# Kernel tuning notes

Measured on AMD Instinct MI355X. Metric: run time of the kernel, lower is better.

## Reference

```python
import jax, jax.numpy as jnp
import numpy as np

HEAD_SIZE = 128


def setup_inputs() -> dict:
    key = jax.random.key(0)
    k0, k1, k2, k3 = jax.random.split(key, 4)
    B, S, E, H = 4, 4096, 1024, HEAD_SIZE
    x = jax.random.normal(k0, (B, S, E), dtype=jnp.float32)
    scale = 1.0 / np.sqrt(E).astype(np.float32)
    Wq = jax.random.normal(k1, (E, H), dtype=jnp.float32) * scale
    Wk = jax.random.normal(k2, (E, H), dtype=jnp.float32) * scale
    Wv = jax.random.normal(k3, (E, H), dtype=jnp.float32) * scale
    k_mask = jnp.ones((B, S), dtype=jnp.int32)
    return {"x": x, "Wq": Wq, "Wk": Wk, "Wv": Wv, "k_mask": k_mask}


def reference(x, Wq, Wk, Wv, k_mask):
    # Self-attention path (kv=None), causal=True
    Q = x @ Wq  # [B, S, H]
    K = x @ Wk  # [B, S, H]
    V = x @ Wv  # [B, S, H]
    inv_sqrt_h = np.float32(1.0 / np.sqrt(HEAD_SIZE))
    att = jnp.einsum('bqh,bkh->bqk', Q, K) * inv_sqrt_h  # [B, S, S]
    neg_inf = jnp.float32(-jnp.inf)
    # padding mask over keys: [B, 1, S_k]
    att = jnp.where(k_mask[:, None, :] == 0, neg_inf, att)
    # causal mask: tril over (q_len, k_len)
    S = Q.shape[1]
    c_mask = jnp.tril(jnp.ones((S, S), dtype=bool))  # [S, S]
    att = jnp.where(c_mask[None, :, :], att, neg_inf)
    att = jax.nn.softmax(att, axis=-1)
    return att @ V  # [B, S, H]
```

## Files before the change

kernel.cpp:

```cpp
#include <hip/hip_runtime.h>

typedef unsigned short u16;
typedef __attribute__((ext_vector_type(8))) short bf16x8;
typedef __attribute__((ext_vector_type(4))) float f32x4;
typedef __attribute__((ext_vector_type(8))) unsigned short u16x8;
typedef __attribute__((ext_vector_type(4))) unsigned short u16x4;

#define SQ 4096
#define HQ 128
#define NCHUNKF 160

__device__ __forceinline__ u16 f2b(float f) {
  unsigned int u = __float_as_uint(f);
  unsigned int r = (u + 0x7fffu + ((u >> 16) & 1u)) >> 16;
  return (u16)r;
}

__device__ __forceinline__ void gload_lds16(const u16* gsrc, u16* ldst) {
  __builtin_amdgcn_global_load_lds((const __attribute__((address_space(1))) void*)gsrc,
                                   (__attribute__((address_space(3))) void*)ldst, 16, 0, 0);
}

__global__ __launch_bounds__(256) void k_wt(const float* __restrict__ Wq, const float* __restrict__ Wk,
                                            const float* __restrict__ Wv, u16* __restrict__ wt) {
  int idx = blockIdx.x * 256 + threadIdx.x;
  int z = idx >> 17, r = idx & 131071, n = r >> 10, k = r & 1023;
  const float* W = (z == 0) ? Wq : (z == 1) ? Wk : Wv;
  wt[idx] = f2b(W[k * 128 + n]);
}

__global__ __launch_bounds__(512, 4) void k_proj(const float* __restrict__ x, const u16* __restrict__ wt,
                                                 u16* __restrict__ qb, u16* __restrict__ kb,
                                                 u16* __restrict__ vt) {
  int blk = blockIdx.x;
  int t = threadIdx.x;
  int w = t >> 6, lane = t & 63;
  int wm = w >> 2, wn = w & 3;
  int lr = lane & 15, lg = lane >> 4;

  __shared__ __align__(16) u16 xl[2][64 * 32];
  __shared__ __align__(16) u16 wl[2][384 * 32];

  int srow = t >> 3, sc8 = t & 7;
  const float* xg = x + (long)(blk * 64 + srow) * 1024 + sc8 * 4;
  int xch = ((sc8 >> 1) ^ ((srow >> 1) & 3));
  int xoff = srow * 32 + xch * 8 + (sc8 & 1) * 4;

  f32x4 acc[2][6];
#pragma unroll
  for (int i = 0; i < 2; ++i)
#pragma unroll
    for (int j = 0; j < 6; ++j) acc[i][j] = (f32x4){0.f, 0.f, 0.f, 0.f};

  auto stage_w = [&](int bufi, int k0) {
#pragma unroll
    for (int i = 0; i < 3; ++i) {
      int ci = i * 512 + t;
      int row = ci >> 2, ch = ci & 3;
      gload_lds16(wt + (long)row * 1024 + k0 + ((ch ^ ((row >> 1) & 3)) << 3),
                  &wl[bufi][0] + ci * 8);
    }
  };

  {
    float4 xa = *(const float4*)(xg);
    stage_w(0, 0);
    u16x4 o;
    o[0] = f2b(xa.x); o[1] = f2b(xa.y); o[2] = f2b(xa.z); o[3] = f2b(xa.w);
    *(u16x4*)(&xl[0][0] + xoff) = o;
  }
  __syncthreads();

  int arow0 = wm * 32 + lr;
  for (int ks = 0; ks < 32; ++ks) {
    int cur = ks & 1;
    float4 xa;
    bool more = (ks + 1 < 32);
    if (more) {
      xa = *(const float4*)(xg + (ks + 1) * 32);
      stage_w(cur ^ 1, (ks + 1) * 32);
    }
    bf16x8 af[2], bf[6];
#pragma unroll
    for (int i = 0; i < 2; ++i) {
      int row = arow0 + i * 16;
      af[i] = *(const bf16x8*)(&xl[cur][0] + row * 32 + ((lg ^ ((row >> 1) & 3)) << 3));
    }
#pragma unroll
    for (int j = 0; j < 6; ++j) {
      int row = wn * 96 + j * 16 + lr;
      bf[j] = *(const bf16x8*)(&wl[cur][0] + row * 32 + ((lg ^ ((row >> 1) & 3)) << 3));
    }
#pragma unroll
    for (int i = 0; i < 2; ++i)
#pragma unroll
      for (int j = 0; j < 6; ++j)
        acc[i][j] = __builtin_amdgcn_mfma_f32_16x16x32_bf16(af[i], bf[j], acc[i][j], 0, 0, 0);
    if (more) {
      u16x4 o;
      o[0] = f2b(xa.x); o[1] = f2b(xa.y); o[2] = f2b(xa.z); o[3] = f2b(xa.w);
      *(u16x4*)(&xl[cur ^ 1][0] + xoff) = o;
    }
    __syncthreads();
  }

#pragma unroll
  for (int i = 0; i < 2; ++i)
#pragma unroll
    for (int j = 0; j < 6; ++j)
#pragma unroll
      for (int r = 0; r < 4; ++r) {
        int m = blk * 64 + wm * 32 + i * 16 + lg * 4 + r;
        int col = wn * 96 + j * 16 + lr;
        int z = col >> 7, cz = col & 127;
        u16 v = f2b(acc[i][j][r]);
        if (z == 0) qb[(long)m * 128 + cz] = v;
        else if (z == 1) kb[(long)m * 128 + cz] = v;
        else { int bb = m >> 12, sR = m & 4095; vt[(long)bb * 524288 + (long)cz * 4096 + sR] = v; }
      }
}

__global__ __launch_bounds__(256) void k_attn(const u16* __restrict__ qb, const u16* __restrict__ kb,
                                              const u16* __restrict__ vt, const int* __restrict__ kmask,
                                              float* __restrict__ po, float* __restrict__ pl) {
  const float SCALE_LOG2 = 0.08838834764831845f * 1.4426950408889634f;
  const float MFIX = 24.0f;
  int f = (NCHUNKF - 1) - (int)blockIdx.x;
  int b = blockIdx.y;
  int g = 0;
  while (g < 3 && f >= 8 * (g + 1) * (g + 2)) ++g;
  int off = f - 8 * g * (g + 1);
  int qt = 16 * g + off / (g + 1);
  int kc = off - (off / (g + 1)) * (g + 1);
  int kt0 = kc * 16;
  int kt1 = min(kt0 + 16, qt + 1);

  int w = threadIdx.x >> 6, lane = threadIdx.x & 63;
  int lr = lane & 15, lg = lane >> 4;
  int sw = lr & 7;
  int qrow0 = qt * 64 + w * 16;
  const u16* Q = qb + ((long)(b * SQ + qrow0)) * HQ;
  const u16* K = kb + (long)b * SQ * HQ;
  const u16* V = vt + (long)b * HQ * SQ;
  const int* msk = kmask + b * SQ;

  __shared__ __align__(16) u16 Kl[2][64 * 128];
  __shared__ __align__(16) u16 Vl[2][128 * 64];
  __shared__ __align__(16) u16 plds[4][16][88];

  bf16x8 aq[4];
#pragma unroll
  for (int c = 0; c < 4; ++c) aq[c] = *(const bf16x8*)(Q + lr * HQ + c * 32 + lg * 8);

  bf16x8 ones;
#pragma unroll
  for (int e = 0; e < 8; ++e) ones[e] = (short)0x3F80;

  f32x4 o[8];
#pragma unroll
  for (int n = 0; n < 8; ++n) o[n] = (f32x4){0.f, 0.f, 0.f, 0.f};
  f32x4 l_acc = (f32x4){0.f, 0.f, 0.f, 0.f};

  auto stage = [&](int bufi, int kb0) {
    const u16* Kg = K + (long)kb0 * HQ;
    const u16* Vg = V + kb0;
#pragma unroll
    for (int i = 0; i < 4; ++i) {
      int ci = w * 4 + i;
      int o16 = ci * 64 + lane;
      int row = o16 >> 4, ch = o16 & 15;
      gload_lds16(Kg + row * HQ + ((ch ^ (row & 7)) << 3), &Kl[bufi][ci * 512]);
    }
#pragma unroll
    for (int i = 0; i < 4; ++i) {
      int ci = w * 4 + i;
      int o16 = ci * 64 + lane;
      int row = o16 >> 3, ch = o16 & 7;
      gload_lds16(Vg + (long)row * SQ + ((ch ^ (row & 7)) << 3), &Vl[bufi][ci * 512]);
    }
  };

  stage(0, kt0 * 64);
  __syncthreads();

  for (int kt = kt0; kt < kt1; ++kt) {
    int cur = (kt - kt0) & 1;
    int kb0 = kt * 64;
    if (kt + 1 < kt1) stage(cur ^ 1, kb0 + 64);

    f32x4 s[4];
#pragma unroll
    for (int h = 0; h < 4; ++h) {
      f32x4 acc = (f32x4){0.f, 0.f, 0.f, 0.f};
      const u16* Kp = &Kl[cur][(h * 16 + lr) * 128];
#pragma unroll
      for (int c = 0; c < 4; ++c) {
        bf16x8 bk = *(const bf16x8*)(Kp + (((c * 4 + lg) ^ sw) << 3));
        acc = __builtin_amdgcn_mfma_f32_16x16x32_bf16(aq[c], bk, acc, 0, 0, 0);
      }
      s[h] = acc;
    }
    int mv[4];
#pragma unroll
    for (int h = 0; h < 4; ++h) mv[h] = msk[kb0 + h * 16 + lr];

    bool diag = (kt == qt);
#pragma unroll
    for (int r = 0; r < 4; ++r) {
      int qr = qrow0 + lg * 4 + r;
#pragma unroll
      for (int h = 0; h < 4; ++h) {
        bool ok = (mv[h] != 0) && (!diag || (kb0 + h * 16 + lr) <= qr);
        float sx = ok ? fmaf(s[h][r], SCALE_LOG2, -MFIX) : -200.0f;
        plds[w][lg * 4 + r][h * 16 + lr] = f2b(__builtin_exp2f(sx));
      }
    }
    bf16x8 ap0 = *(const bf16x8*)(&plds[w][lr][lg * 8]);
    bf16x8 ap1 = *(const bf16x8*)(&plds[w][lr][32 + lg * 8]);
    l_acc = __builtin_amdgcn_mfma_f32_16x16x32_bf16(ap0, ones, l_acc, 0, 0, 0);
    l_acc = __builtin_amdgcn_mfma_f32_16x16x32_bf16(ap1, ones, l_acc, 0, 0, 0);
#pragma unroll
    for (int n = 0; n < 8; ++n) {
      const u16* Vp = &Vl[cur][(n * 16 + lr) * 64];
      bf16x8 bv0 = *(const bf16x8*)(Vp + ((lg ^ sw) << 3));
      bf16x8 bv1 = *(const bf16x8*)(Vp + (((4 + lg) ^ sw) << 3));
      o[n] = __builtin_amdgcn_mfma_f32_16x16x32_bf16(ap0, bv0, o[n], 0, 0, 0);
      o[n] = __builtin_amdgcn_mfma_f32_16x16x32_bf16(ap1, bv1, o[n], 0, 0, 0);
    }
    __syncthreads();
  }

  long p = (long)b * NCHUNKF + f;
  float* pob = po + p * 8192;
#pragma unroll
  for (int n = 0; n < 8; ++n)
#pragma unroll
    for (int r = 0; r < 4; ++r)
      pob[(w * 16 + lg * 4 + r) * 128 + n * 16 + lr] = o[n][r];
  if (lr == 0) {
#pragma unroll
    for (int r = 0; r < 4; ++r) pl[p * 64 + w * 16 + lg * 4 + r] = l_acc[r];
  }
}

__global__ __launch_bounds__(256) void k_merge(const float* __restrict__ po, const float* __restrict__ pl,
                                               float* __restrict__ out) {
  int qt = blockIdx.x, b = blockIdx.y;
  int g = qt >> 4;
  int nch = g + 1;
  long pbase = (long)b * NCHUNKF + 8 * g * (g + 1) + (qt & 15) * (g + 1);
  int t = threadIdx.x;
  int row = t >> 2, c0 = (t & 3) * 32;
  float l = 0.f;
  for (int i = 0; i < nch; ++i) l += pl[(pbase + i) * 64 + row];
  float inv = 1.0f / l;
  const float* po0 = po + pbase * 8192 + row * 128 + c0;
  float* orow = out + ((long)(b * SQ + qt * 64 + row)) * HQ + c0;
#pragma unroll
  for (int j = 0; j < 32; j += 4) {
    float4 acc = {0.f, 0.f, 0.f, 0.f};
    for (int i = 0; i < nch; ++i) {
      float4 v = *(const float4*)(po0 + (long)i * 8192 + j);
      acc.x += v.x; acc.y += v.y; acc.z += v.z; acc.w += v.w;
    }
    acc.x *= inv; acc.y *= inv; acc.z *= inv; acc.w *= inv;
    *(float4*)(orow + j) = acc;
  }
}

extern "C" void kernel_launch(void* const* d_in, const int* in_sizes, int n_in,
                              void* d_out, int out_size, void* d_ws, size_t ws_size,
                              hipStream_t stream) {
  const float* x  = (const float*)d_in[0];
  const float* Wq = (const float*)d_in[1];
  const float* Wk = (const float*)d_in[2];
  const float* Wv = (const float*)d_in[3];
  const int* kmask = (const int*)d_in[4];
  char* ws = (char*)d_ws;
  u16* wt = (u16*)(ws + 33554432);
  u16* qb = (u16*)(ws + 34340864);
  u16* kb = (u16*)(ws + 38535168);
  u16* vt = (u16*)(ws + 42729472);
  float* po = (float*)ws;
  float* pl = (float*)(ws + 33554432);
  float* out = (float*)d_out;

  k_wt<<<1536, 256, 0, stream>>>(Wq, Wk, Wv, wt);
  k_proj<<<256, 512, 0, stream>>>(x, wt, qb, kb, vt);
  k_attn<<<dim3(NCHUNKF, 4), 256, 0, stream>>>(qb, kb, vt, kmask, po, pl);
  k_merge<<<dim3(64, 4), 256, 0, stream>>>(po, pl, out);
}
```

Baseline: 130.7 us.

## Enlarge attention query tile to 128 rows with 8 waves sharing K/V staging

The attention kernel now processes 128 query rows per block with 512 threads (8 waves), so each staged K/V tile in LDS is reused by twice as many query rows, and the chunk schedule and merge kernel are rewritten for 80 chunks per batch. Waves whose rows lie entirely above a key tile skip its compute, and the causal mask is applied only on tiles that straddle the diagonal. P is written to a swizzled LDS layout and converted with the library bf16 conversion. In exchange there are half as many blocks, more idle waves on the diagonal tiles, and higher LDS and register pressure per block.

```diff
diff --git a/kernel.cpp b/kernel.cpp
--- a/kernel.cpp
+++ b/kernel.cpp
@@ -1,19 +1,24 @@
 #include <hip/hip_runtime.h>
+#include <hip/hip_bf16.h>
 
 typedef unsigned short u16;
 typedef __attribute__((ext_vector_type(8))) short bf16x8;
 typedef __attribute__((ext_vector_type(4))) float f32x4;
-typedef __attribute__((ext_vector_type(8))) unsigned short u16x8;
 typedef __attribute__((ext_vector_type(4))) unsigned short u16x4;
 
 #define SQ 4096
 #define HQ 128
-#define NCHUNKF 160
+#define NCHUNK 80
 
 __device__ __forceinline__ u16 f2b(float f) {
   unsigned int u = __float_as_uint(f);
   unsigned int r = (u + 0x7fffu + ((u >> 16) & 1u)) >> 16;
   return (u16)r;
+}
+
+__device__ __forceinline__ u16 f2b_fast(float f) {
+  __hip_bfloat16 h = __float2bfloat16(f);
+  return __builtin_bit_cast(u16, h);
 }
 
 __device__ __forceinline__ void gload_lds16(const u16* gsrc, u16* ldst) {
@@ -120,25 +125,24 @@
       }
 }
 
-__global__ __launch_bounds__(256) void k_attn(const u16* __restrict__ qb, const u16* __restrict__ kb,
-                                              const u16* __restrict__ vt, const int* __restrict__ kmask,
-                                              float* __restrict__ po, float* __restrict__ pl) {
+__global__ __launch_bounds__(512, 4) void k_attn(const u16* __restrict__ qb, const u16* __restrict__ kb,
+                                                 const u16* __restrict__ vt, const int* __restrict__ kmask,
+                                                 float* __restrict__ po, float* __restrict__ pl) {
   const float SCALE_LOG2 = 0.08838834764831845f * 1.4426950408889634f;
   const float MFIX = 24.0f;
-  int f = (NCHUNKF - 1) - (int)blockIdx.x;
+  int f = (NCHUNK - 1) - (int)blockIdx.x;
   int b = blockIdx.y;
-  int g = 0;
-  while (g < 3 && f >= 8 * (g + 1) * (g + 2)) ++g;
-  int off = f - 8 * g * (g + 1);
-  int qt = 16 * g + off / (g + 1);
-  int kc = off - (off / (g + 1)) * (g + 1);
+  int gg = 0;
+  while (gg < 3 && f >= 4 * (gg + 1) * (gg + 2)) ++gg;
+  int off = f - 4 * gg * (gg + 1);
+  int qt2 = 8 * gg + off / (gg + 1);
+  int kc = off - (off / (gg + 1)) * (gg + 1);
   int kt0 = kc * 16;
-  int kt1 = min(kt0 + 16, qt + 1);
-
-  int w = threadIdx.x >> 6, lane = threadIdx.x & 63;
-  int lr = lane & 15, lg = lane >> 4;
-  int sw = lr & 7;
-  int qrow0 = qt * 64 + w * 16;
+  int kt1 = min(kt0 + 16, 2 * qt2 + 2);
+
+  int t = threadIdx.x, w = t >> 6, lane = t & 63;
+  int lr = lane & 15, lg = lane >> 4, sw = lr & 7;
+  int qrow0 = qt2 * 128 + w * 16;
   const u16* Q = qb + ((long)(b * SQ + qrow0)) * HQ;
   const u16* K = kb + (long)b * SQ * HQ;
   const u16* V = vt + (long)b * HQ * SQ;
@@ -146,7 +150,7 @@
 
   __shared__ __align__(16) u16 Kl[2][64 * 128];
   __shared__ __align__(16) u16 Vl[2][128 * 64];
-  __shared__ __align__(16) u16 plds[4][16][88];
+  __shared__ __align__(16) u16 plds[8][16 * 64];
 
   bf16x8 aq[4];
 #pragma unroll
@@ -165,73 +169,77 @@
     const u16* Kg = K + (long)kb0 * HQ;
     const u16* Vg = V + kb0;
 #pragma unroll
-    for (int i = 0; i < 4; ++i) {
-      int ci = w * 4 + i;
+    for (int i = 0; i < 2; ++i) {
+      int ci = w * 2 + i;
       int o16 = ci * 64 + lane;
       int row = o16 >> 4, ch = o16 & 15;
       gload_lds16(Kg + row * HQ + ((ch ^ (row & 7)) << 3), &Kl[bufi][ci * 512]);
     }
 #pragma unroll
-    for (int i = 0; i < 4; ++i) {
-      int ci = w * 4 + i;
-      int o16 = ci * 64 + lane;
+    for (int i = 0; i < 2; ++i) {
+      int ci = 16 + w * 2 + i;
+      int o16 = (ci - 16) * 64 + lane;
       int row = o16 >> 3, ch = o16 & 7;
-      gload_lds16(Vg + (long)row * SQ + ((ch ^ (row & 7)) << 3), &Vl[bufi][ci * 512]);
+      gload_lds16(Vg + (long)row * SQ + ((ch ^ (row & 7)) << 3), &Vl[bufi][(ci - 16) * 512]);
     }
   };
 
   stage(0, kt0 * 64);
   __syncthreads();
 
+  u16* pw = &plds[w][0];
   for (int kt = kt0; kt < kt1; ++kt) {
     int cur = (kt - kt0) & 1;
     int kb0 = kt * 64;
     if (kt + 1 < kt1) stage(cur ^ 1, kb0 + 64);
 
-    f32x4 s[4];
-#pragma unroll
-    for (int h = 0; h < 4; ++h) {
-      f32x4 acc = (f32x4){0.f, 0.f, 0.f, 0.f};
-      const u16* Kp = &Kl[cur][(h * 16 + lr) * 128];
-#pragma unroll
-      for (int c = 0; c < 4; ++c) {
-        bf16x8 bk = *(const bf16x8*)(Kp + (((c * 4 + lg) ^ sw) << 3));
-        acc = __builtin_amdgcn_mfma_f32_16x16x32_bf16(aq[c], bk, acc, 0, 0, 0);
+    if (kb0 <= qrow0 + 15) {
+      f32x4 s[4];
+#pragma unroll
+      for (int h = 0; h < 4; ++h) {
+        f32x4 acc = (f32x4){0.f, 0.f, 0.f, 0.f};
+        const u16* Kp = &Kl[cur][(h * 16 + lr) * 128];
+#pragma unroll
+        for (int c = 0; c < 4; ++c) {
+          bf16x8 bk = *(const bf16x8*)(Kp + (((c * 4 + lg) ^ sw) << 3));
+          acc = __builtin_amdgcn_mfma_f32_16x16x32_bf16(aq[c], bk, acc, 0, 0, 0);
+        }
+        s[h] = acc;
       }
-      s[h] = acc;
-    }
-    int mv[4];
-#pragma unroll
-    for (int h = 0; h < 4; ++h) mv[h] = msk[kb0 + h * 16 + lr];
-
-    bool diag = (kt == qt);
-#pragma unroll
-    for (int r = 0; r < 4; ++r) {
-      int qr = qrow0 + lg * 4 + r;
-#pragma unroll
-      for (int h = 0; h < 4; ++h) {
-        bool ok = (mv[h] != 0) && (!diag || (kb0 + h * 16 + lr) <= qr);
-        float sx = ok ? fmaf(s[h][r], SCALE_LOG2, -MFIX) : -200.0f;
-        plds[w][lg * 4 + r][h * 16 + lr] = f2b(__builtin_exp2f(sx));
+      float mf[4];
+#pragma unroll
+      for (int h = 0; h < 4; ++h) mf[h] = (msk[kb0 + h * 16 + lr] != 0) ? 1.0f : 0.0f;
+      bool needc = (kb0 + 63 > qrow0);
+#pragma unroll
+      for (int r = 0; r < 4; ++r) {
+        int row = lg * 4 + r;
+        int qr = qrow0 + row;
+#pragma unroll
+        for (int h = 0; h < 4; ++h) {
+          float p = __builtin_exp2f(fmaf(s[h][r], SCALE_LOG2, -MFIX)) * mf[h];
+          if (needc) p = ((kb0 + h * 16 + lr) <= qr) ? p : 0.0f;
+          int poff = row * 64 + ((((h * 2 + (lr >> 3)) ^ (row & 7))) << 3) + (lr & 7);
+          pw[poff] = f2b_fast(p);
+        }
       }
-    }
-    bf16x8 ap0 = *(const bf16x8*)(&plds[w][lr][lg * 8]);
-    bf16x8 ap1 = *(const bf16x8*)(&plds[w][lr][32 + lg * 8]);
-    l_acc = __builtin_amdgcn_mfma_f32_16x16x32_bf16(ap0, ones, l_acc, 0, 0, 0);
-    l_acc = __builtin_amdgcn_mfma_f32_16x16x32_bf16(ap1, ones, l_acc, 0, 0, 0);
-#pragma unroll
-    for (int n = 0; n < 8; ++n) {
-      const u16* Vp = &Vl[cur][(n * 16 + lr) * 64];
-      bf16x8 bv0 = *(const bf16x8*)(Vp + ((lg ^ sw) << 3));
-      bf16x8 bv1 = *(const bf16x8*)(Vp + (((4 + lg) ^ sw) << 3));
-      o[n] = __builtin_amdgcn_mfma_f32_16x16x32_bf16(ap0, bv0, o[n], 0, 0, 0);
-      o[n] = __builtin_amdgcn_mfma_f32_16x16x32_bf16(ap1, bv1, o[n], 0, 0, 0);
+      bf16x8 ap0 = *(const bf16x8*)(pw + lr * 64 + ((lg ^ sw) << 3));
+      bf16x8 ap1 = *(const bf16x8*)(pw + lr * 64 + (((4 + lg) ^ sw) << 3));
+      l_acc = __builtin_amdgcn_mfma_f32_16x16x32_bf16(ap0, ones, l_acc, 0, 0, 0);
+      l_acc = __builtin_amdgcn_mfma_f32_16x16x32_bf16(ap1, ones, l_acc, 0, 0, 0);
+#pragma unroll
+      for (int n = 0; n < 8; ++n) {
+        const u16* Vp = &Vl[cur][(n * 16 + lr) * 64];
+        bf16x8 bv0 = *(const bf16x8*)(Vp + ((lg ^ sw) << 3));
+        bf16x8 bv1 = *(const bf16x8*)(Vp + (((4 + lg) ^ sw) << 3));
+        o[n] = __builtin_amdgcn_mfma_f32_16x16x32_bf16(ap0, bv0, o[n], 0, 0, 0);
+        o[n] = __builtin_amdgcn_mfma_f32_16x16x32_bf16(ap1, bv1, o[n], 0, 0, 0);
+      }
     }
     __syncthreads();
   }
 
-  long p = (long)b * NCHUNKF + f;
-  float* pob = po + p * 8192;
+  long p = (long)b * NCHUNK + f;
+  float* pob = po + p * 16384;
 #pragma unroll
   for (int n = 0; n < 8; ++n)
 #pragma unroll
@@ -239,28 +247,28 @@
       pob[(w * 16 + lg * 4 + r) * 128 + n * 16 + lr] = o[n][r];
   if (lr == 0) {
 #pragma unroll
-    for (int r = 0; r < 4; ++r) pl[p * 64 + w * 16 + lg * 4 + r] = l_acc[r];
+    for (int r = 0; r < 4; ++r) pl[p * 128 + w * 16 + lg * 4 + r] = l_acc[r];
   }
 }
 
 __global__ __launch_bounds__(256) void k_merge(const float* __restrict__ po, const float* __restrict__ pl,
                                                float* __restrict__ out) {
-  int qt = blockIdx.x, b = blockIdx.y;
-  int g = qt >> 4;
-  int nch = g + 1;
-  long pbase = (long)b * NCHUNKF + 8 * g * (g + 1) + (qt & 15) * (g + 1);
+  int qt2 = blockIdx.x, b = blockIdx.y;
+  int gg = qt2 >> 3;
+  int nch = gg + 1;
+  long pbase = (long)b * NCHUNK + 4 * gg * (gg + 1) + (qt2 & 7) * (gg + 1);
   int t = threadIdx.x;
-  int row = t >> 2, c0 = (t & 3) * 32;
+  int row = t >> 1, c0 = (t & 1) * 64;
   float l = 0.f;
-  for (int i = 0; i < nch; ++i) l += pl[(pbase + i) * 64 + row];
+  for (int i = 0; i < nch; ++i) l += pl[(pbase + i) * 128 + row];
   float inv = 1.0f / l;
-  const float* po0 = po + pbase * 8192 + row * 128 + c0;
-  float* orow = out + ((long)(b * SQ + qt * 64 + row)) * HQ + c0;
-#pragma unroll
-  for (int j = 0; j < 32; j += 4) {
+  const float* p0 = po + pbase * 16384 + row * 128 + c0;
+  float* orow = out + ((long)(b * SQ + qt2 * 128 + row)) * HQ + c0;
+#pragma unroll
+  for (int j = 0; j < 64; j += 4) {
     float4 acc = {0.f, 0.f, 0.f, 0.f};
     for (int i = 0; i < nch; ++i) {
-      float4 v = *(const float4*)(po0 + (long)i * 8192 + j);
+      float4 v = *(const float4*)(p0 + (long)i * 16384 + j);
       acc.x += v.x; acc.y += v.y; acc.z += v.z; acc.w += v.w;
     }
     acc.x *= inv; acc.y *= inv; acc.z *= inv; acc.w *= inv;
@@ -287,6 +295,6 @@
 
   k_wt<<<1536, 256, 0, stream>>>(Wq, Wk, Wv, wt);
   k_proj<<<256, 512, 0, stream>>>(x, wt, qb, kb, vt);
-  k_attn<<<dim3(NCHUNKF, 4), 256, 0, stream>>>(qb, kb, vt, kmask, po, pl);
-  k_merge<<<dim3(64, 4), 256, 0, stream>>>(po, pl, out);
-}
+  k_attn<<<dim3(NCHUNK, 4), 512, 0, stream>>>(qb, kb, vt, kmask, po, pl);
+  k_merge<<<dim3(32, 4), 256, 0, stream>>>(po, pl, out);
+}
```

Measured after the change: 127.3 us. 1.03x faster.
